# Kernel tuning notes

Hardware: AMD Instinct MI355X
Metric: run time of the kernel (lower is better)

Reference implementation:

```python
import jax, jax.numpy as jnp
import numpy as np

DIM = 1024
N_EXPERTS = 8
TOP_K = 2
B, S = 2, 1024


def setup_inputs() -> dict:
    key = jax.random.key(0)
    ks = jax.random.split(key, 4)
    scale = 0.02
    return {
        "u_t": jax.random.normal(ks[0], (B, S, DIM), dtype=jnp.float32),
        "centroids": jax.random.normal(ks[1], (N_EXPERTS, DIM), dtype=jnp.float32),
        "score_biases": jnp.zeros((N_EXPERTS,), dtype=jnp.float32),
        "W1": jax.random.normal(ks[2], (N_EXPERTS, DIM, 4 * DIM), dtype=jnp.float32) * scale,
        "b1": jnp.zeros((N_EXPERTS, 4 * DIM), dtype=jnp.float32),
        "W2": jax.random.normal(ks[3], (N_EXPERTS, 4 * DIM, DIM), dtype=jnp.float32) * scale,
        "b2": jnp.zeros((N_EXPERTS, DIM), dtype=jnp.float32),
    }


def reference(u_t, centroids, score_biases, W1, b1, W2, b2):
    Bs, Ss, dim = u_t.shape
    T = Bs * Ss
    N = centroids.shape[0]
    K = TOP_K

    u_flat = u_t.reshape(T, dim)
    scores = u_flat @ centroids.T + score_biases          # [T, N]
    gate = jax.nn.softmax(scores, axis=-1)                # [T, N]
    topk_vals, topk_idx = jax.lax.top_k(gate, K)          # [T, K]

    flat_idx = topk_idx.reshape(-1)                       # [T*K]

    # load-violation stats (no grad path; pure counts)
    perfect_load = K * T / N
    f_i = jnp.zeros((N,), dtype=jnp.float32).at[flat_idx].add(1.0)
    maxvio = (jnp.max(f_i) - perfect_load) / perfect_load

    # Grouped MLP expressed as dense per-expert compute over all tokens,
    # then combined with a sparse [T, N] gate matrix (same math as masked dispatch).
    h = jax.nn.relu(jnp.einsum("td,ndh->nth", u_flat, W1) + b1[:, None, :])  # [N, T, 4*dim]
    expert_outs = jnp.einsum("nth,nhd->ntd", h, W2) + b2[:, None, :]          # [N, T, dim]

    rows = jnp.repeat(jnp.arange(T), K)
    combine_w = jnp.zeros((T, N), dtype=topk_vals.dtype).at[rows, flat_idx].add(topk_vals.reshape(-1))
    out = jnp.einsum("tn,ntd->td", combine_w, expert_outs).reshape(Bs, Ss, dim)
    return (out, maxvio)
```

## Files before the change

kernel.cpp:

```cpp
#include <hip/hip_runtime.h>
#include <hip/hip_bf16.h>

#define T_TOK 2048
#define DIMS  1024
#define HID   4096
#define NE    8

typedef __bf16 bf16x8 __attribute__((ext_vector_type(8)));
typedef float  f32x4  __attribute__((ext_vector_type(4)));

__device__ __forceinline__ unsigned short f2bf(float f) {
  unsigned u = __float_as_uint(f);
  u += 0x7FFFu + ((u >> 16) & 1u);
  return (unsigned short)(u >> 16);
}
__device__ __forceinline__ float bf2f(unsigned short s) {
  return __uint_as_float(((unsigned)s) << 16);
}

__device__ __forceinline__ void g2l16(const void* g, void* l) {
  __builtin_amdgcn_global_load_lds((const __attribute__((address_space(1))) void*)g,
                                   (__attribute__((address_space(3))) void*)l,
                                   16, 0, 0);
}

__global__ __launch_bounds__(256) void k_route(const float* __restrict__ u,
    const float* __restrict__ cent, const float* __restrict__ sbias,
    int* __restrict__ topk_idx, float* __restrict__ topk_val,
    unsigned short* __restrict__ ub) {
  int wave = threadIdx.x >> 6;
  int lane = threadIdx.x & 63;
  int t = blockIdx.x * 4 + wave;
  const float* ur = u + (size_t)t * DIMS;
  float p[NE];
#pragma unroll
  for (int n = 0; n < NE; n++) p[n] = 0.f;
#pragma unroll
  for (int ch = 0; ch < 4; ch++) {
    int d = ch * 256 + lane * 4;
    float4 uv = *(const float4*)(ur + d);
    ushort4 o4;
    o4.x = f2bf(uv.x); o4.y = f2bf(uv.y); o4.z = f2bf(uv.z); o4.w = f2bf(uv.w);
    *(ushort4*)(ub + (size_t)t * DIMS + d) = o4;
#pragma unroll
    for (int n = 0; n < NE; n++) {
      float4 cv = *(const float4*)(cent + n * DIMS + d);
      p[n] += uv.x * cv.x + uv.y * cv.y + uv.z * cv.z + uv.w * cv.w;
    }
  }
#pragma unroll
  for (int n = 0; n < NE; n++) {
#pragma unroll
    for (int o = 32; o > 0; o >>= 1) p[n] += __shfl_xor(p[n], o);
  }
  if (lane == 0) {
    float g[NE];
    float m = -1e30f;
#pragma unroll
    for (int n = 0; n < NE; n++) { g[n] = p[n] + sbias[n]; m = fmaxf(m, g[n]); }
    float sum = 0.f;
#pragma unroll
    for (int n = 0; n < NE; n++) { g[n] = expf(g[n] - m); sum += g[n]; }
    float inv = 1.f / sum;
#pragma unroll
    for (int n = 0; n < NE; n++) g[n] *= inv;
    int i0 = 0;
#pragma unroll
    for (int n = 1; n < NE; n++) if (g[n] > g[i0]) i0 = n;
    int i1 = (i0 == 0) ? 1 : 0;
#pragma unroll
    for (int n = 0; n < NE; n++) if (n != i0 && g[n] > g[i1]) i1 = n;
    topk_idx[2 * t] = i0;     topk_idx[2 * t + 1] = i1;
    topk_val[2 * t] = g[i0];  topk_val[2 * t + 1] = g[i1];
  }
}

__global__ __launch_bounds__(256) void k_finalize(const int* __restrict__ topk_idx,
    int* __restrict__ cnt, int* __restrict__ offs, int* __restrict__ cursor,
    float* __restrict__ maxvio) {
  __shared__ int lc[NE];
  if (threadIdx.x < NE) lc[threadIdx.x] = 0;
  __syncthreads();
#pragma unroll
  for (int i = 0; i < 16; i++) {
    int e = topk_idx[threadIdx.x * 16 + i];
    atomicAdd(&lc[e], 1);
  }
  __syncthreads();
  if (threadIdx.x == 0) {
    int o = 0, mx = 0;
#pragma unroll
    for (int n = 0; n < NE; n++) {
      int c = lc[n];
      cnt[n] = c; offs[n] = o; cursor[n] = 0;
      o += c; mx = max(mx, c);
    }
    maxvio[0] = ((float)mx - 512.f) / 512.f;
  }
}

__global__ __launch_bounds__(256) void k_place(const int* __restrict__ topk_idx,
    const int* __restrict__ offs, int* __restrict__ cursor,
    int* __restrict__ rowtok, int* __restrict__ pairpos) {
  int t = blockIdx.x * 256 + threadIdx.x;
  if (t >= T_TOK) return;
#pragma unroll
  for (int k = 0; k < 2; k++) {
    int e = topk_idx[2 * t + k];
    int pos = atomicAdd(&cursor[e], 1);
    rowtok[offs[e] + pos] = t;
    pairpos[2 * t + k] = offs[e] + pos;
  }
}

#define BM 128
#define BN 128
#define BK 64

__global__ __launch_bounds__(256) void k_gemm1(const unsigned short* __restrict__ ub,
    const float* __restrict__ W1, const float* __restrict__ b1,
    const int* __restrict__ rowtok, const int* __restrict__ cnts, const int* __restrict__ offs,
    unsigned short* __restrict__ h) {
  int e = blockIdx.z;
  int cnt = cnts[e];
  int m0 = blockIdx.y * BM;
  if (m0 >= cnt) return;
  int off = offs[e];
  int n0 = blockIdx.x * BN;
  __shared__ __align__(16) unsigned char smem[32768];

  int tid = threadIdx.x;
  int lane = tid & 63;
  int wv = tid >> 6;
  int wm = (tid >> 7) & 1;
  int wn = (tid >> 6) & 1;
  int srow = tid >> 3;
  int cp = tid & 7;
  const float* w1e = W1 + (size_t)e * DIMS * HID;
  const unsigned short* gA[2];
#pragma unroll
  for (int a = 0; a < 2; a++) {
    int r = a * 64 + (srow & 31) + ((tid >> 8) << 5);
    (void)r;
  }
  const unsigned short* gAp[4];
#pragma unroll
  for (int a = 0; a < 4; a++) {
    int r = a * 32 + srow;
    int c = cp ^ (r & 7);
    int pr = min(off + m0 + r, off + cnt - 1);
    int tok = rowtok[pr];
    gAp[a] = ub + (size_t)tok * DIMS + c * 8;
  }
  int wboff = __builtin_amdgcn_readfirstlane(wv << 10);
  f32x4 acc[4][4];
  f32x4 zz = {0.f, 0.f, 0.f, 0.f};
#pragma unroll
  for (int i = 0; i < 4; i++)
#pragma unroll
    for (int j = 0; j < 4; j++) acc[i][j] = zz;

  int lane15 = lane & 15, quad = lane >> 4, l7 = lane & 7;
  unsigned aRowOff = (unsigned)((wm * 64 + lane15) * 128);
  unsigned bRowOff = (unsigned)(16384 + (wn * 64 + lane15) * 128);
  int csB = 0;

#pragma unroll 1
  for (int k0 = 0; k0 < DIMS; k0 += BK) {
#pragma unroll
    for (int a = 0; a < 4; a++) g2l16(gAp[a] + k0, smem + a * 4096 + wboff);
#pragma unroll
    for (int jj = 0; jj < 4; jj++) {
      int j = wv * 4 + jj;
      int kc = j & 7, nh = j >> 3;
      int nloc = nh * 64 + lane;
      const float* src = w1e + (size_t)(k0 + kc * 8) * HID + n0 + nloc;
      float t0, t1, t2, t3, t4, t5, t6, t7;
      t0 = src[0];            t1 = src[(size_t)HID];
      t2 = src[(size_t)2 * HID]; t3 = src[(size_t)3 * HID];
      t4 = src[(size_t)4 * HID]; t5 = src[(size_t)5 * HID];
      t6 = src[(size_t)6 * HID]; t7 = src[(size_t)7 * HID];
      bf16x8 pk;
      pk[0] = (__bf16)t0; pk[1] = (__bf16)t1; pk[2] = (__bf16)t2; pk[3] = (__bf16)t3;
      pk[4] = (__bf16)t4; pk[5] = (__bf16)t5; pk[6] = (__bf16)t6; pk[7] = (__bf16)t7;
      csB = kc ^ (lane & 7);
      *(bf16x8*)(smem + 16384 + nloc * 128 + csB * 16) = pk;
    }
    __syncthreads();
#pragma unroll
    for (int s = 0; s < 2; s++) {
      unsigned cpf = (unsigned)(((s * 4 + quad) ^ l7) * 16);
      bf16x8 af[4], bfr[4];
#pragma unroll
      for (int i = 0; i < 4; i++) af[i] = *(const bf16x8*)(smem + aRowOff + i * 2048 + cpf);
#pragma unroll
      for (int j = 0; j < 4; j++) bfr[j] = *(const bf16x8*)(smem + bRowOff + j * 2048 + cpf);
#pragma unroll
      for (int i = 0; i < 4; i++)
#pragma unroll
        for (int j = 0; j < 4; j++)
          acc[i][j] = __builtin_amdgcn_mfma_f32_16x16x32_bf16(af[i], bfr[j], acc[i][j], 0, 0, 0);
    }
    __syncthreads();
  }
  float b1v[4];
#pragma unroll
  for (int j = 0; j < 4; j++) b1v[j] = b1[e * HID + n0 + wn * 64 + j * 16 + lane15];
#pragma unroll
  for (int i = 0; i < 4; i++) {
#pragma unroll
    for (int r = 0; r < 4; r++) {
      int mrow = m0 + wm * 64 + i * 16 + quad * 4 + r;
      if (mrow < cnt) {
        size_t hrow = (size_t)(off + mrow) * HID;
#pragma unroll
        for (int j = 0; j < 4; j++) {
          int col = n0 + wn * 64 + j * 16 + lane15;
          float v = fmaxf(acc[i][j][r] + b1v[j], 0.f);
          h[hrow + col] = f2bf(v);
        }
      }
    }
  }
}

__global__ __launch_bounds__(256) void k_gemm2(const unsigned short* __restrict__ hbuf,
    const float* __restrict__ W2, const float* __restrict__ b2,
    const int* __restrict__ cnts, const int* __restrict__ offs,
    unsigned short* __restrict__ pout, int KC) {
  int z = blockIdx.z;
  int e = z & 7;
  int sp = z >> 3;
  int cnt = cnts[e];
  int m0 = blockIdx.y * BM;
  if (m0 >= cnt) return;
  int off = offs[e];
  int n0 = blockIdx.x * BN;
  __shared__ __align__(16) unsigned char smem[32768];

  int tid = threadIdx.x;
  int lane = tid & 63;
  int wv = tid >> 6;
  int wm = (tid >> 7) & 1;
  int wn = (tid >> 6) & 1;
  int srow = tid >> 3;
  int cp = tid & 7;
  const float* w2e = W2 + (size_t)e * HID * DIMS;
  const unsigned short* gAp[4];
#pragma unroll
  for (int a = 0; a < 4; a++) {
    int r = a * 32 + srow;
    int c = cp ^ (r & 7);
    int pr = min(off + m0 + r, off + cnt - 1);
    gAp[a] = hbuf + (size_t)pr * HID + c * 8;
  }
  int wboff = __builtin_amdgcn_readfirstlane(wv << 10);
  f32x4 acc[4][4];
  f32x4 zz = {0.f, 0.f, 0.f, 0.f};
#pragma unroll
  for (int i = 0; i < 4; i++)
#pragma unroll
    for (int j = 0; j < 4; j++) acc[i][j] = zz;

  int lane15 = lane & 15, quad = lane >> 4, l7 = lane & 7;
  unsigned aRowOff = (unsigned)((wm * 64 + lane15) * 128);
  unsigned bRowOff = (unsigned)(16384 + (wn * 64 + lane15) * 128);

  int kbeg = sp * KC, kend = kbeg + KC;
#pragma unroll 1
  for (int k0 = kbeg; k0 < kend; k0 += BK) {
#pragma unroll
    for (int a = 0; a < 4; a++) g2l16(gAp[a] + k0, smem + a * 4096 + wboff);
#pragma unroll
    for (int jj = 0; jj < 4; jj++) {
      int j = wv * 4 + jj;
      int kc = j & 7, nh = j >> 3;
      int nloc = nh * 64 + lane;
      const float* src = w2e + (size_t)(k0 + kc * 8) * DIMS + n0 + nloc;
      float t0, t1, t2, t3, t4, t5, t6, t7;
      t0 = src[0];             t1 = src[(size_t)DIMS];
      t2 = src[(size_t)2 * DIMS]; t3 = src[(size_t)3 * DIMS];
      t4 = src[(size_t)4 * DIMS]; t5 = src[(size_t)5 * DIMS];
      t6 = src[(size_t)6 * DIMS]; t7 = src[(size_t)7 * DIMS];
      bf16x8 pk;
      pk[0] = (__bf16)t0; pk[1] = (__bf16)t1; pk[2] = (__bf16)t2; pk[3] = (__bf16)t3;
      pk[4] = (__bf16)t4; pk[5] = (__bf16)t5; pk[6] = (__bf16)t6; pk[7] = (__bf16)t7;
      int cs = kc ^ (lane & 7);
      *(bf16x8*)(smem + 16384 + nloc * 128 + cs * 16) = pk;
    }
    __syncthreads();
#pragma unroll
    for (int s = 0; s < 2; s++) {
      unsigned cpf = (unsigned)(((s * 4 + quad) ^ l7) * 16);
      bf16x8 af[4], bfr[4];
#pragma unroll
      for (int i = 0; i < 4; i++) af[i] = *(const bf16x8*)(smem + aRowOff + i * 2048 + cpf);
#pragma unroll
      for (int j = 0; j < 4; j++) bfr[j] = *(const bf16x8*)(smem + bRowOff + j * 2048 + cpf);
#pragma unroll
      for (int i = 0; i < 4; i++)
#pragma unroll
        for (int j = 0; j < 4; j++)
          acc[i][j] = __builtin_amdgcn_mfma_f32_16x16x32_bf16(af[i], bfr[j], acc[i][j], 0, 0, 0);
    }
    __syncthreads();
  }
  float b2v[4];
#pragma unroll
  for (int j = 0; j < 4; j++)
    b2v[j] = (sp == 0) ? b2[e * DIMS + n0 + wn * 64 + j * 16 + lane15] : 0.f;
  unsigned short* pme = pout + (size_t)sp * T_TOK * 2 * DIMS;
#pragma unroll
  for (int i = 0; i < 4; i++) {
#pragma unroll
    for (int r = 0; r < 4; r++) {
      int mrow = m0 + wm * 64 + i * 16 + quad * 4 + r;
      if (mrow < cnt) {
        size_t prow = (size_t)(off + mrow) * DIMS;
#pragma unroll
        for (int j = 0; j < 4; j++) {
          int col = n0 + wn * 64 + j * 16 + lane15;
          pme[prow + col] = f2bf(acc[i][j][r] + b2v[j]);
        }
      }
    }
  }
}

__global__ __launch_bounds__(256) void k_combine(const unsigned short* __restrict__ pout,
    const int* __restrict__ pairpos, const float* __restrict__ tkv,
    float* __restrict__ out, int nsplit) {
  int t = blockIdx.x;
  int d = threadIdx.x * 4;
  int p0 = pairpos[2 * t], p1 = pairpos[2 * t + 1];
  float w0 = tkv[2 * t], w1 = tkv[2 * t + 1];
  float a0 = 0.f, a1 = 0.f, a2 = 0.f, a3 = 0.f;
  float c0 = 0.f, c1 = 0.f, c2 = 0.f, c3 = 0.f;
  const size_t SS = (size_t)T_TOK * 2 * DIMS;
  for (int s = 0; s < nsplit; s++) {
    ushort4 av = *(const ushort4*)(pout + s * SS + (size_t)p0 * DIMS + d);
    ushort4 bv = *(const ushort4*)(pout + s * SS + (size_t)p1 * DIMS + d);
    a0 += bf2f(av.x); a1 += bf2f(av.y); a2 += bf2f(av.z); a3 += bf2f(av.w);
    c0 += bf2f(bv.x); c1 += bf2f(bv.y); c2 += bf2f(bv.z); c3 += bf2f(bv.w);
  }
  float4 o;
  o.x = w0 * a0 + w1 * c0;
  o.y = w0 * a1 + w1 * c1;
  o.z = w0 * a2 + w1 * c2;
  o.w = w0 * a3 + w1 * c3;
  *(float4*)(out + (size_t)t * DIMS + d) = o;
}

extern "C" void kernel_launch(void* const* d_in, const int* in_sizes, int n_in,
                              void* d_out, int out_size, void* d_ws, size_t ws_size,
                              hipStream_t stream) {
  const float* u     = (const float*)d_in[0];
  const float* cent  = (const float*)d_in[1];
  const float* sbias = (const float*)d_in[2];
  const float* W1    = (const float*)d_in[3];
  const float* b1    = (const float*)d_in[4];
  const float* W2    = (const float*)d_in[5];
  const float* b2    = (const float*)d_in[6];
  float* out = (float*)d_out;

  char* ws = (char*)d_ws;
  unsigned short* ubuf = (unsigned short*)(ws);
  unsigned short* hbuf = (unsigned short*)(ws + 4194304);
  const size_t POUT_OFF = 37748736ull;
  const size_t PSZ = (size_t)T_TOK * 2 * DIMS * 2;
  int nsplit = (ws_size >= POUT_OFF + 4 * PSZ + (1u << 20)) ? 4 : 1;
  unsigned short* poutb = (unsigned short*)(ws + POUT_OFF);
  char* r = ws + POUT_OFF + (size_t)nsplit * PSZ;
  int*   cnt      = (int*)(r);
  int*   offs     = (int*)(r + 64);
  int*   cursor   = (int*)(r + 128);
  int*   topk_idx = (int*)(r + 256);
  float* topk_val = (float*)(r + 256 + 16384);
  int*   rowtok   = (int*)(r + 256 + 32768);
  int*   pairpos  = (int*)(r + 256 + 49152);

  k_route<<<512, 256, 0, stream>>>(u, cent, sbias, topk_idx, topk_val, ubuf);
  k_finalize<<<1, 256, 0, stream>>>(topk_idx, cnt, offs, cursor, out + 2097152);
  k_place<<<8, 256, 0, stream>>>(topk_idx, offs, cursor, rowtok, pairpos);
  k_gemm1<<<dim3(32, 16, 8), 256, 0, stream>>>(ubuf, W1, b1, rowtok, cnt, offs, hbuf);
  k_gemm2<<<dim3(8, 16, 8 * nsplit), 256, 0, stream>>>(hbuf, W2, b2, cnt, offs,
                                                       poutb, HID / nsplit);
  k_combine<<<2048, 256, 0, stream>>>(poutb, pairpos, topk_val, out, nsplit);
}
```

Before: 427.8 us.

## Prefetch next K-tile into registers to overlap global loads with MFMA

Both expert GEMM kernels now load the next K-tile's activation rows and fp32 weights into registers before running the MFMA work on the current shared-memory tile, then convert and store them after a barrier. This aims to hide global-load latency behind matrix compute instead of stalling at the start of each iteration. Launch bounds request two blocks per SM, which limits registers while the register footprint grows with 32 prefetched floats plus 4 uint4 per thread, so spills or lower occupancy are possible. The A tile now goes through registers rather than the direct global-to-LDS load, except for the first tile.

```diff
diff --git a/kernel.cpp b/kernel.cpp
--- a/kernel.cpp
+++ b/kernel.cpp
@@ -117,7 +117,7 @@
 #define BN 128
 #define BK 64
 
-__global__ __launch_bounds__(256) void k_gemm1(const unsigned short* __restrict__ ub,
+__global__ __launch_bounds__(256, 2) void k_gemm1(const unsigned short* __restrict__ ub,
     const float* __restrict__ W1, const float* __restrict__ b1,
     const int* __restrict__ rowtok, const int* __restrict__ cnts, const int* __restrict__ offs,
     unsigned short* __restrict__ h) {
@@ -137,12 +137,6 @@
   int srow = tid >> 3;
   int cp = tid & 7;
   const float* w1e = W1 + (size_t)e * DIMS * HID;
-  const unsigned short* gA[2];
-#pragma unroll
-  for (int a = 0; a < 2; a++) {
-    int r = a * 64 + (srow & 31) + ((tid >> 8) << 5);
-    (void)r;
-  }
   const unsigned short* gAp[4];
 #pragma unroll
   for (int a = 0; a < 4; a++) {
@@ -152,7 +146,19 @@
     int tok = rowtok[pr];
     gAp[a] = ub + (size_t)tok * DIMS + c * 8;
   }
+  const float* gBp[4];
+  int csw[4], nlv[4];
+#pragma unroll
+  for (int jj = 0; jj < 4; jj++) {
+    int j = wv * 4 + jj;
+    int kc = j & 7, nh = j >> 3;
+    int nloc = nh * 64 + lane;
+    nlv[jj] = nloc;
+    csw[jj] = kc ^ (lane & 7);
+    gBp[jj] = w1e + (size_t)(kc * 8) * HID + n0 + nloc;
+  }
   int wboff = __builtin_amdgcn_readfirstlane(wv << 10);
+  unsigned aWr = (unsigned)(wboff + lane * 16);
   f32x4 acc[4][4];
   f32x4 zz = {0.f, 0.f, 0.f, 0.f};
 #pragma unroll
@@ -163,30 +169,42 @@
   int lane15 = lane & 15, quad = lane >> 4, l7 = lane & 7;
   unsigned aRowOff = (unsigned)((wm * 64 + lane15) * 128);
   unsigned bRowOff = (unsigned)(16384 + (wn * 64 + lane15) * 128);
-  int csB = 0;
+
+#pragma unroll
+  for (int a = 0; a < 4; a++) g2l16(gAp[a], smem + a * 4096 + wboff);
+  {
+    float bp[32];
+#pragma unroll
+    for (int jj = 0; jj < 4; jj++) {
+      const float* src = gBp[jj];
+#pragma unroll
+      for (int i = 0; i < 8; i++) bp[jj * 8 + i] = src[(size_t)i * HID];
+    }
+#pragma unroll
+    for (int jj = 0; jj < 4; jj++) {
+      bf16x8 pk;
+#pragma unroll
+      for (int i = 0; i < 8; i++) pk[i] = (__bf16)bp[jj * 8 + i];
+      *(bf16x8*)(smem + 16384 + nlv[jj] * 128 + csw[jj] * 16) = pk;
+    }
+  }
+  __syncthreads();
 
 #pragma unroll 1
   for (int k0 = 0; k0 < DIMS; k0 += BK) {
-#pragma unroll
-    for (int a = 0; a < 4; a++) g2l16(gAp[a] + k0, smem + a * 4096 + wboff);
-#pragma unroll
-    for (int jj = 0; jj < 4; jj++) {
-      int j = wv * 4 + jj;
-      int kc = j & 7, nh = j >> 3;
-      int nloc = nh * 64 + lane;
-      const float* src = w1e + (size_t)(k0 + kc * 8) * HID + n0 + nloc;
-      float t0, t1, t2, t3, t4, t5, t6, t7;
-      t0 = src[0];            t1 = src[(size_t)HID];
-      t2 = src[(size_t)2 * HID]; t3 = src[(size_t)3 * HID];
-      t4 = src[(size_t)4 * HID]; t5 = src[(size_t)5 * HID];
-      t6 = src[(size_t)6 * HID]; t7 = src[(size_t)7 * HID];
-      bf16x8 pk;
-      pk[0] = (__bf16)t0; pk[1] = (__bf16)t1; pk[2] = (__bf16)t2; pk[3] = (__bf16)t3;
-      pk[4] = (__bf16)t4; pk[5] = (__bf16)t5; pk[6] = (__bf16)t6; pk[7] = (__bf16)t7;
-      csB = kc ^ (lane & 7);
-      *(bf16x8*)(smem + 16384 + nloc * 128 + csB * 16) = pk;
-    }
-    __syncthreads();
+    int kn = k0 + BK;
+    uint4 apre[4];
+    float bp[32];
+    if (kn < DIMS) {
+#pragma unroll
+      for (int a = 0; a < 4; a++) apre[a] = *(const uint4*)(gAp[a] + kn);
+#pragma unroll
+      for (int jj = 0; jj < 4; jj++) {
+        const float* src = gBp[jj] + (size_t)kn * HID;
+#pragma unroll
+        for (int i = 0; i < 8; i++) bp[jj * 8 + i] = src[(size_t)i * HID];
+      }
+    }
 #pragma unroll
     for (int s = 0; s < 2; s++) {
       unsigned cpf = (unsigned)(((s * 4 + quad) ^ l7) * 16);
@@ -202,6 +220,18 @@
           acc[i][j] = __builtin_amdgcn_mfma_f32_16x16x32_bf16(af[i], bfr[j], acc[i][j], 0, 0, 0);
     }
     __syncthreads();
+    if (kn < DIMS) {
+#pragma unroll
+      for (int a = 0; a < 4; a++) *(uint4*)(smem + a * 4096 + aWr) = apre[a];
+#pragma unroll
+      for (int jj = 0; jj < 4; jj++) {
+        bf16x8 pk;
+#pragma unroll
+        for (int i = 0; i < 8; i++) pk[i] = (__bf16)bp[jj * 8 + i];
+        *(bf16x8*)(smem + 16384 + nlv[jj] * 128 + csw[jj] * 16) = pk;
+      }
+      __syncthreads();
+    }
   }
   float b1v[4];
 #pragma unroll
@@ -224,7 +254,7 @@
   }
 }
 
-__global__ __launch_bounds__(256) void k_gemm2(const unsigned short* __restrict__ hbuf,
+__global__ __launch_bounds__(256, 2) void k_gemm2(const unsigned short* __restrict__ hbuf,
     const float* __restrict__ W2, const float* __restrict__ b2,
     const int* __restrict__ cnts, const int* __restrict__ offs,
     unsigned short* __restrict__ pout, int KC) {
@@ -254,7 +284,19 @@
     int pr = min(off + m0 + r, off + cnt - 1);
     gAp[a] = hbuf + (size_t)pr * HID + c * 8;
   }
+  const float* gBp[4];
+  int csw[4], nlv[4];
+#pragma unroll
+  for (int jj = 0; jj < 4; jj++) {
+    int j = wv * 4 + jj;
+    int kc = j & 7, nh = j >> 3;
+    int nloc = nh * 64 + lane;
+    nlv[jj] = nloc;
+    csw[jj] = kc ^ (lane & 7);
+    gBp[jj] = w2e + (size_t)(kc * 8) * DIMS + n0 + nloc;
+  }
   int wboff = __builtin_amdgcn_readfirstlane(wv << 10);
+  unsigned aWr = (unsigned)(wboff + lane * 16);
   f32x4 acc[4][4];
   f32x4 zz = {0.f, 0.f, 0.f, 0.f};
 #pragma unroll
@@ -267,28 +309,41 @@
   unsigned bRowOff = (unsigned)(16384 + (wn * 64 + lane15) * 128);
 
   int kbeg = sp * KC, kend = kbeg + KC;
+#pragma unroll
+  for (int a = 0; a < 4; a++) g2l16(gAp[a] + kbeg, smem + a * 4096 + wboff);
+  {
+    float bp[32];
+#pragma unroll
+    for (int jj = 0; jj < 4; jj++) {
+      const float* src = gBp[jj] + (size_t)kbeg * DIMS;
+#pragma unroll
+      for (int i = 0; i < 8; i++) bp[jj * 8 + i] = src[(size_t)i * DIMS];
+    }
+#pragma unroll
+    for (int jj = 0; jj < 4; jj++) {
+      bf16x8 pk;
+#pragma unroll
+      for (int i = 0; i < 8; i++) pk[i] = (__bf16)bp[jj * 8 + i];
+      *(bf16x8*)(smem + 16384 + nlv[jj] * 128 + csw[jj] * 16) = pk;
+    }
+  }
+  __syncthreads();
+
 #pragma unroll 1
   for (int k0 = kbeg; k0 < kend; k0 += BK) {
-#pragma unroll
-    for (int a = 0; a < 4; a++) g2l16(gAp[a] + k0, smem + a * 4096 + wboff);
-#pragma unroll
-    for (int jj = 0; jj < 4; jj++) {
-      int j = wv * 4 + jj;
-      int kc = j & 7, nh = j >> 3;
-      int nloc = nh * 64 + lane;
-      const float* src = w2e + (size_t)(k0 + kc * 8) * DIMS + n0 + nloc;
-      float t0, t1, t2, t3, t4, t5, t6, t7;
-      t0 = src[0];             t1 = src[(size_t)DIMS];
-      t2 = src[(size_t)2 * DIMS]; t3 = src[(size_t)3 * DIMS];
-      t4 = src[(size_t)4 * DIMS]; t5 = src[(size_t)5 * DIMS];
-      t6 = src[(size_t)6 * DIMS]; t7 = src[(size_t)7 * DIMS];
-      bf16x8 pk;
-      pk[0] = (__bf16)t0; pk[1] = (__bf16)t1; pk[2] = (__bf16)t2; pk[3] = (__bf16)t3;
-      pk[4] = (__bf16)t4; pk[5] = (__bf16)t5; pk[6] = (__bf16)t6; pk[7] = (__bf16)t7;
-      int cs = kc ^ (lane & 7);
-      *(bf16x8*)(smem + 16384 + nloc * 128 + cs * 16) = pk;
-    }
-    __syncthreads();
+    int kn = k0 + BK;
+    uint4 apre[4];
+    float bp[32];
+    if (kn < kend) {
+#pragma unroll
+      for (int a = 0; a < 4; a++) apre[a] = *(const uint4*)(gAp[a] + kn);
+#pragma unroll
+      for (int jj = 0; jj < 4; jj++) {
+        const float* src = gBp[jj] + (size_t)kn * DIMS;
+#pragma unroll
+        for (int i = 0; i < 8; i++) bp[jj * 8 + i] = src[(size_t)i * DIMS];
+      }
+    }
 #pragma unroll
     for (int s = 0; s < 2; s++) {
       unsigned cpf = (unsigned)(((s * 4 + quad) ^ l7) * 16);
@@ -304,6 +359,18 @@
           acc[i][j] = __builtin_amdgcn_mfma_f32_16x16x32_bf16(af[i], bfr[j], acc[i][j], 0, 0, 0);
     }
     __syncthreads();
+    if (kn < kend) {
+#pragma unroll
+      for (int a = 0; a < 4; a++) *(uint4*)(smem + a * 4096 + aWr) = apre[a];
+#pragma unroll
+      for (int jj = 0; jj < 4; jj++) {
+        bf16x8 pk;
+#pragma unroll
+        for (int i = 0; i < 8; i++) pk[i] = (__bf16)bp[jj * 8 + i];
+        *(bf16x8*)(smem + 16384 + nlv[jj] * 128 + csw[jj] * 16) = pk;
+      }
+      __syncthreads();
+    }
   }
   float b2v[4];
 #pragma unroll
```

Measured after the change: 558.4 us. 1.31x slower.
